# Kernel optimization log

Hardware: AMD Instinct MI355X
Metric: run time of the kernel (lower is better)

Reference implementation:

```python
import jax, jax.numpy as jnp
import numpy as np

B, H, L, D, BLK = 2, 16, 2048, 64, 32
NB = L // BLK          # 64 blocks per side
WINDOW = 8             # causal local window, in blocks


def make_layout():
    # [H, NB, NB] int32: block (i, j) active iff 0 <= i - j < WINDOW (causal local band)
    bi = jnp.arange(NB)
    band = ((bi[:, None] - bi[None, :]) >= 0) & ((bi[:, None] - bi[None, :]) < WINDOW)
    return jnp.broadcast_to(band[None].astype(jnp.int32), (H, NB, NB))


def setup_inputs() -> dict:
    rng = jax.random.key(0)
    kq, kk, kv, kp = jax.random.split(rng, 4)
    return {
        "query": jax.random.normal(kq, (B, H, L, D), dtype=jnp.float32),
        "key": jax.random.normal(kk, (B, H, L, D), dtype=jnp.float32),
        "value": jax.random.normal(kv, (B, H, L, D), dtype=jnp.float32),
        "key_padding_mask": jax.random.normal(kp, (B, L), dtype=jnp.float32),
        "layout": make_layout(),
    }


def reference(query, key, value, key_padding_mask, layout):
    # query/key/value: [B, H, L, D]; layout: [H, NB, NB] block sparsity pattern
    bsz, num_heads, tgt_len, head_dim = query.shape
    blk = tgt_len // layout.shape[1]
    scaling = float(head_dim) ** (-0.5)

    # SDD: scores only on active blocks. Reference computes dense then masks
    # inactive blocks to -inf, matching blocksparse softmax semantics exactly.
    scores = jnp.einsum("bhqd,bhkd->bhqk", query, key) * scaling
    # key_padding_mask_mode='add': added to logits, broadcast over queries
    scores = scores + key_padding_mask[:, None, None, :]

    # expand block layout [H, NB, NB] -> element mask [H, L, L]
    block_mask = jnp.repeat(jnp.repeat(layout.astype(bool), blk, axis=1), blk, axis=2)
    scores = jnp.where(block_mask[None], scores, -jnp.inf)

    probs = jax.nn.softmax(scores, axis=-1)  # zeros outside active blocks
    # DSD: probs @ value
    attn_output = jnp.einsum("bhqk,bhkd->bhqd", probs, value)
    return attn_output
```

## Files before the change

### kernel.cpp

```cpp
#include <hip/hip_runtime.h>

#define B_   2
#define H_   16
#define L_   2048
#define D_   64
#define BLK_ 32
#define NB_  64
#define WIN_ 8

#define KS 72
#define VS 40
#define PS 40

typedef __bf16 bf16x8 __attribute__((ext_vector_type(8)));
typedef float  f32x4  __attribute__((ext_vector_type(4)));
typedef unsigned short u16x4 __attribute__((ext_vector_type(4)));
typedef unsigned short u16x8 __attribute__((ext_vector_type(8)));

__device__ inline unsigned short f2bf(float f) {
    unsigned int u = __builtin_bit_cast(unsigned int, f);
    unsigned int r = u + 0x7fffu + ((u >> 16) & 1u);
    return (unsigned short)(r >> 16);
}

__global__ __launch_bounds__(256, 4)
void sparse_attn_kernel(const float* __restrict__ qg,
                        const float* __restrict__ kg,
                        const float* __restrict__ vg,
                        const float* __restrict__ kpm,
                        const int*   __restrict__ layout,
                        float* __restrict__ outg)
{
    __shared__ __align__(16) unsigned short Ks_[2][BLK_ * KS];
    __shared__ __align__(16) unsigned short Vt_[2][D_ * VS];
    __shared__ __align__(16) unsigned short Ps_[4][16 * PS];

    const int tid  = threadIdx.x;
    const int wave = tid >> 6;
    const int lane = tid & 63;
    const int quad = lane >> 4;
    const int l15  = lane & 15;

    const int phys = blockIdx.x;
    const int lw   = (phys & 7) * 128 + (phys >> 3);
    const int ip = lw & 31;
    const int h  = (lw >> 5) & 15;
    const int b  = lw >> 9;
    const int i0 = ip * 2, i1 = i0 + 1;
    const int iq = i0 + (wave >> 1);

    const size_t bh = (size_t)(b * H_ + h);
    const float* kbase  = kg  + bh * L_ * D_;
    const float* vbase  = vg  + bh * L_ * D_;
    const float* kpb    = kpm + (size_t)b * L_;
    const int*   layrow = layout + (h * NB_ + iq) * NB_;

    bf16x8 aq[2];
    {
        const int gq = iq * BLK_ + (wave & 1) * 16 + l15;
        const float* qrow = qg + (bh * L_ + gq) * D_;
        #pragma unroll
        for (int ks = 0; ks < 2; ++ks) {
            float4 x = *(const float4*)&qrow[ks * 32 + quad * 8];
            float4 y = *(const float4*)&qrow[ks * 32 + quad * 8 + 4];
            u16x8 pk;
            pk[0]=f2bf(x.x); pk[1]=f2bf(x.y); pk[2]=f2bf(x.z); pk[3]=f2bf(x.w);
            pk[4]=f2bf(y.x); pk[5]=f2bf(y.y); pk[6]=f2bf(y.z); pk[7]=f2bf(y.w);
            aq[ks] = __builtin_bit_cast(bf16x8, pk);
        }
    }

    int jlo = i0 - (WIN_ - 1);
    if (jlo < 0) jlo = 0;

    {
        const float4* kb = (const float4*)(kbase + (size_t)jlo * BLK_ * D_);
        float4 a0 = kb[tid];
        float4 a1 = kb[tid + 256];
        const float* vb = vbase + (size_t)jlo * BLK_ * D_;
        float vr[8];
        #pragma unroll
        for (int i = 0; i < 8; ++i) vr[i] = vb[(wave * 8 + i) * D_ + lane];
        {
            int row = tid >> 4, c4 = tid & 15;
            u16x4 pk; pk[0]=f2bf(a0.x); pk[1]=f2bf(a0.y); pk[2]=f2bf(a0.z); pk[3]=f2bf(a0.w);
            *(u16x4*)&Ks_[0][row * KS + c4 * 4] = pk;
            int f4 = tid + 256; row = f4 >> 4; c4 = f4 & 15;
            u16x4 pj; pj[0]=f2bf(a1.x); pj[1]=f2bf(a1.y); pj[2]=f2bf(a1.z); pj[3]=f2bf(a1.w);
            *(u16x4*)&Ks_[0][row * KS + c4 * 4] = pj;
        }
        {
            u16x8 pv;
            #pragma unroll
            for (int i = 0; i < 8; ++i) pv[i] = f2bf(vr[i]);
            *(u16x8*)&Vt_[0][lane * VS + ((wave ^ (lane & 3)) * 8)] = pv;
        }
    }
    float kp0c = kpb[jlo * BLK_ + l15];
    float kp1c = kpb[jlo * BLK_ + 16 + l15];
    __syncthreads();

    float lrow[4] = {0.f, 0.f, 0.f, 0.f};
    f32x4 Ot[4];
    #pragma unroll
    for (int t = 0; t < 4; ++t) Ot[t] = (f32x4){0.f, 0.f, 0.f, 0.f};

    int cur = 0;
    for (int j = jlo; j <= i1; ++j) {
        const bool havenext = (j < i1);
        float4 kr0, kr1; float vr[8];
        float kp0n = 0.f, kp1n = 0.f;
        if (havenext) {
            const float4* kb = (const float4*)(kbase + (size_t)(j + 1) * BLK_ * D_);
            kr0 = kb[tid]; kr1 = kb[tid + 256];
            const float* vb = vbase + (size_t)(j + 1) * BLK_ * D_;
            #pragma unroll
            for (int i = 0; i < 8; ++i) vr[i] = vb[(wave * 8 + i) * D_ + lane];
            kp0n = kpb[(j + 1) * BLK_ + l15];
            kp1n = kpb[(j + 1) * BLK_ + 16 + l15];
        }

        if (layrow[j] != 0) {
            f32x4 s0 = {0.f,0.f,0.f,0.f}, s1 = {0.f,0.f,0.f,0.f};
            #pragma unroll
            for (int ks = 0; ks < 2; ++ks) {
                bf16x8 b0 = *(const bf16x8*)&Ks_[cur][l15 * KS + ks * 32 + quad * 8];
                bf16x8 b1 = *(const bf16x8*)&Ks_[cur][(16 + l15) * KS + ks * 32 + quad * 8];
                s0 = __builtin_amdgcn_mfma_f32_16x16x32_bf16(aq[ks], b0, s0, 0, 0, 0);
                s1 = __builtin_amdgcn_mfma_f32_16x16x32_bf16(aq[ks], b1, s1, 0, 0, 0);
            }
            unsigned short* psw = &Ps_[wave][0];
            #pragma unroll
            for (int r = 0; r < 4; ++r) {
                float v0 = s0[r] * 0.125f + kp0c;
                float v1 = s1[r] * 0.125f + kp1c;
                float p0 = __expf(v0);
                float p1 = __expf(v1);
                lrow[r] += p0 + p1;
                int prow = quad * 4 + r;
                psw[prow * PS + l15]      = f2bf(p0);
                psw[prow * PS + 16 + l15] = f2bf(p1);
            }
            asm volatile("s_waitcnt lgkmcnt(0)" ::: "memory");
            bf16x8 ap = *(const bf16x8*)&psw[l15 * PS + quad * 8];
            #pragma unroll
            for (int t = 0; t < 4; ++t) {
                bf16x8 bv = *(const bf16x8*)&Vt_[cur][(t * 16 + l15) * VS + ((quad ^ (l15 & 3)) * 8)];
                Ot[t] = __builtin_amdgcn_mfma_f32_16x16x32_bf16(ap, bv, Ot[t], 0, 0, 0);
            }
        }

        if (havenext) {
            const int nb = cur ^ 1;
            int row = tid >> 4, c4 = tid & 15;
            u16x4 pk; pk[0]=f2bf(kr0.x); pk[1]=f2bf(kr0.y); pk[2]=f2bf(kr0.z); pk[3]=f2bf(kr0.w);
            *(u16x4*)&Ks_[nb][row * KS + c4 * 4] = pk;
            int f4 = tid + 256; row = f4 >> 4; c4 = f4 & 15;
            u16x4 pj; pj[0]=f2bf(kr1.x); pj[1]=f2bf(kr1.y); pj[2]=f2bf(kr1.z); pj[3]=f2bf(kr1.w);
            *(u16x4*)&Ks_[nb][row * KS + c4 * 4] = pj;
            u16x8 pv;
            #pragma unroll
            for (int i = 0; i < 8; ++i) pv[i] = f2bf(vr[i]);
            *(u16x8*)&Vt_[nb][lane * VS + ((wave ^ (lane & 3)) * 8)] = pv;
            kp0c = kp0n; kp1c = kp1n;
        }
        __syncthreads();
        cur ^= 1;
    }

    #pragma unroll
    for (int r = 0; r < 4; ++r) {
        #pragma unroll
        for (int m = 1; m < 16; m <<= 1) lrow[r] += __shfl_xor(lrow[r], m);
    }
    float* ob = outg + (bh * L_ + (size_t)iq * BLK_ + (wave & 1) * 16) * D_;
    #pragma unroll
    for (int r = 0; r < 4; ++r) {
        float inv = 1.0f / lrow[r];
        int prow = quad * 4 + r;
        #pragma unroll
        for (int t = 0; t < 4; ++t)
            ob[prow * D_ + t * 16 + l15] = Ot[t][r] * inv;
    }
}

extern "C" void kernel_launch(void* const* d_in, const int* in_sizes, int n_in,
                              void* d_out, int out_size, void* d_ws, size_t ws_size,
                              hipStream_t stream) {
    const float* q      = (const float*)d_in[0];
    const float* k      = (const float*)d_in[1];
    const float* v      = (const float*)d_in[2];
    const float* kpmask = (const float*)d_in[3];
    const int*   layout = (const int*)d_in[4];
    float* out = (float*)d_out;

    dim3 grid(B_ * H_ * (NB_ / 2));
    dim3 block(256);
    sparse_attn_kernel<<<grid, block, 0, stream>>>(q, k, v, kpmask, layout, out);
}
```

Before: 105.6 us.

## Fully unroll fixed 9-step block loop with two-deep register prefetch and XOR-swizzled K

```diff
diff --git a/kernel.cpp b/kernel.cpp
--- a/kernel.cpp
+++ b/kernel.cpp
@@ -6,15 +6,13 @@
 #define D_   64
 #define BLK_ 32
 #define NB_  64
-#define WIN_ 8
 
-#define KS 72
-#define VS 40
-#define PS 40
+#define KSW 64
+#define VS  40
+#define PS  40
 
 typedef __bf16 bf16x8 __attribute__((ext_vector_type(8)));
 typedef float  f32x4  __attribute__((ext_vector_type(4)));
-typedef unsigned short u16x4 __attribute__((ext_vector_type(4)));
 typedef unsigned short u16x8 __attribute__((ext_vector_type(8)));
 
 __device__ inline unsigned short f2bf(float f) {
@@ -22,6 +20,14 @@
     unsigned int r = u + 0x7fffu + ((u >> 16) & 1u);
     return (unsigned short)(r >> 16);
 }
+
+#define WG_BARRIER() asm volatile("s_waitcnt lgkmcnt(0)\n\ts_barrier" ::: "memory")
+
+struct Tile {
+    float4 k0, k1;
+    float  v[8];
+    float  kp0, kp1;
+};
 
 __global__ __launch_bounds__(256, 4)
 void sparse_attn_kernel(const float* __restrict__ qg,
@@ -31,7 +37,7 @@
                         const int*   __restrict__ layout,
                         float* __restrict__ outg)
 {
-    __shared__ __align__(16) unsigned short Ks_[2][BLK_ * KS];
+    __shared__ __align__(16) unsigned short Ks_[2][BLK_ * KSW];
     __shared__ __align__(16) unsigned short Vt_[2][D_ * VS];
     __shared__ __align__(16) unsigned short Ps_[4][16 * PS];
 
@@ -55,6 +61,15 @@
     const float* kpb    = kpm + (size_t)b * L_;
     const int*   layrow = layout + (h * NB_ + iq) * NB_;
 
+    const int jbeg = i0 - 7;
+
+    int act[9];
+    #pragma unroll
+    for (int s = 0; s < 9; ++s) {
+        const int j = jbeg + s;
+        act[s] = (j >= 0) ? layrow[j] : 0;
+    }
+
     bf16x8 aq[2];
     {
         const int gq = iq * BLK_ + (wave & 1) * 16 + l15;
@@ -70,101 +85,84 @@
         }
     }
 
-    int jlo = i0 - (WIN_ - 1);
-    if (jlo < 0) jlo = 0;
+    auto clampj = [&](int j) { return j < 0 ? 0 : j; };
 
-    {
-        const float4* kb = (const float4*)(kbase + (size_t)jlo * BLK_ * D_);
-        float4 a0 = kb[tid];
-        float4 a1 = kb[tid + 256];
-        const float* vb = vbase + (size_t)jlo * BLK_ * D_;
-        float vr[8];
+    auto loadT = [&](int jc, Tile& T) {
+        const float4* kb = (const float4*)(kbase + (size_t)jc * BLK_ * D_);
+        T.k0 = kb[tid * 2];
+        T.k1 = kb[tid * 2 + 1];
+        const float* vb = vbase + (size_t)jc * BLK_ * D_;
         #pragma unroll
-        for (int i = 0; i < 8; ++i) vr[i] = vb[(wave * 8 + i) * D_ + lane];
-        {
-            int row = tid >> 4, c4 = tid & 15;
-            u16x4 pk; pk[0]=f2bf(a0.x); pk[1]=f2bf(a0.y); pk[2]=f2bf(a0.z); pk[3]=f2bf(a0.w);
-            *(u16x4*)&Ks_[0][row * KS + c4 * 4] = pk;
-            int f4 = tid + 256; row = f4 >> 4; c4 = f4 & 15;
-            u16x4 pj; pj[0]=f2bf(a1.x); pj[1]=f2bf(a1.y); pj[2]=f2bf(a1.z); pj[3]=f2bf(a1.w);
-            *(u16x4*)&Ks_[0][row * KS + c4 * 4] = pj;
-        }
-        {
-            u16x8 pv;
-            #pragma unroll
-            for (int i = 0; i < 8; ++i) pv[i] = f2bf(vr[i]);
-            *(u16x8*)&Vt_[0][lane * VS + ((wave ^ (lane & 3)) * 8)] = pv;
-        }
-    }
-    float kp0c = kpb[jlo * BLK_ + l15];
-    float kp1c = kpb[jlo * BLK_ + 16 + l15];
-    __syncthreads();
+        for (int i = 0; i < 8; ++i) T.v[i] = vb[(wave * 8 + i) * D_ + lane];
+        T.kp0 = kpb[jc * BLK_ + l15];
+        T.kp1 = kpb[jc * BLK_ + 16 + l15];
+    };
+
+    auto storeT = [&](int buf, const Tile& T) {
+        const int row = tid >> 3, oct = tid & 7;
+        u16x8 pk;
+        pk[0]=f2bf(T.k0.x); pk[1]=f2bf(T.k0.y); pk[2]=f2bf(T.k0.z); pk[3]=f2bf(T.k0.w);
+        pk[4]=f2bf(T.k1.x); pk[5]=f2bf(T.k1.y); pk[6]=f2bf(T.k1.z); pk[7]=f2bf(T.k1.w);
+        *(u16x8*)&Ks_[buf][row * KSW + ((oct ^ (row & 7)) * 8)] = pk;
+        u16x8 pv;
+        #pragma unroll
+        for (int i = 0; i < 8; ++i) pv[i] = f2bf(T.v[i]);
+        *(u16x8*)&Vt_[buf][lane * VS + ((wave ^ (lane & 3)) * 8)] = pv;
+    };
 
     float lrow[4] = {0.f, 0.f, 0.f, 0.f};
     f32x4 Ot[4];
     #pragma unroll
     for (int t = 0; t < 4; ++t) Ot[t] = (f32x4){0.f, 0.f, 0.f, 0.f};
 
+    auto computeT = [&](int buf, float kp0c, float kp1c) {
+        f32x4 s0 = {0.f,0.f,0.f,0.f}, s1 = {0.f,0.f,0.f,0.f};
+        #pragma unroll
+        for (int ks = 0; ks < 2; ++ks) {
+            const int so = ((ks * 4 + quad) ^ (l15 & 7)) * 8;
+            bf16x8 b0 = *(const bf16x8*)&Ks_[buf][l15 * KSW + so];
+            bf16x8 b1 = *(const bf16x8*)&Ks_[buf][(16 + l15) * KSW + so];
+            s0 = __builtin_amdgcn_mfma_f32_16x16x32_bf16(aq[ks], b0, s0, 0, 0, 0);
+            s1 = __builtin_amdgcn_mfma_f32_16x16x32_bf16(aq[ks], b1, s1, 0, 0, 0);
+        }
+        unsigned short* psw = &Ps_[wave][0];
+        #pragma unroll
+        for (int r = 0; r < 4; ++r) {
+            float p0 = __expf(s0[r] * 0.125f + kp0c);
+            float p1 = __expf(s1[r] * 0.125f + kp1c);
+            lrow[r] += p0 + p1;
+            const int prow = quad * 4 + r;
+            psw[prow * PS + l15]      = f2bf(p0);
+            psw[prow * PS + 16 + l15] = f2bf(p1);
+        }
+        asm volatile("s_waitcnt lgkmcnt(0)" ::: "memory");
+        bf16x8 ap = *(const bf16x8*)&psw[l15 * PS + quad * 8];
+        #pragma unroll
+        for (int t = 0; t < 4; ++t) {
+            bf16x8 bv = *(const bf16x8*)&Vt_[buf][(t * 16 + l15) * VS + ((quad ^ (l15 & 3)) * 8)];
+            Ot[t] = __builtin_amdgcn_mfma_f32_16x16x32_bf16(ap, bv, Ot[t], 0, 0, 0);
+        }
+    };
+
+    Tile tiles[2];
+    loadT(clampj(jbeg), tiles[0]);
+    storeT(0, tiles[0]);
+    float kp0c = tiles[0].kp0, kp1c = tiles[0].kp1;
+    loadT(clampj(jbeg + 1), tiles[1]);
+    WG_BARRIER();
+
     int cur = 0;
-    for (int j = jlo; j <= i1; ++j) {
-        const bool havenext = (j < i1);
-        float4 kr0, kr1; float vr[8];
-        float kp0n = 0.f, kp1n = 0.f;
-        if (havenext) {
-            const float4* kb = (const float4*)(kbase + (size_t)(j + 1) * BLK_ * D_);
-            kr0 = kb[tid]; kr1 = kb[tid + 256];
-            const float* vb = vbase + (size_t)(j + 1) * BLK_ * D_;
-            #pragma unroll
-            for (int i = 0; i < 8; ++i) vr[i] = vb[(wave * 8 + i) * D_ + lane];
-            kp0n = kpb[(j + 1) * BLK_ + l15];
-            kp1n = kpb[(j + 1) * BLK_ + 16 + l15];
+    #pragma unroll
+    for (int s = 0; s < 9; ++s) {
+        const int j = jbeg + s;
+        if (s <= 6) loadT(clampj(j + 2), tiles[s & 1]);
+        if (act[s] != 0) computeT(cur, kp0c, kp1c);
+        if (s < 8) {
+            const Tile& T = tiles[(s + 1) & 1];
+            storeT(cur ^ 1, T);
+            kp0c = T.kp0; kp1c = T.kp1;
         }
-
-        if (layrow[j] != 0) {
-            f32x4 s0 = {0.f,0.f,0.f,0.f}, s1 = {0.f,0.f,0.f,0.f};
-            #pragma unroll
-            for (int ks = 0; ks < 2; ++ks) {
-                bf16x8 b0 = *(const bf16x8*)&Ks_[cur][l15 * KS + ks * 32 + quad * 8];
-                bf16x8 b1 = *(const bf16x8*)&Ks_[cur][(16 + l15) * KS + ks * 32 + quad * 8];
-                s0 = __builtin_amdgcn_mfma_f32_16x16x32_bf16(aq[ks], b0, s0, 0, 0, 0);
-                s1 = __builtin_amdgcn_mfma_f32_16x16x32_bf16(aq[ks], b1, s1, 0, 0, 0);
-            }
-            unsigned short* psw = &Ps_[wave][0];
-            #pragma unroll
-            for (int r = 0; r < 4; ++r) {
-                float v0 = s0[r] * 0.125f + kp0c;
-                float v1 = s1[r] * 0.125f + kp1c;
-                float p0 = __expf(v0);
-                float p1 = __expf(v1);
-                lrow[r] += p0 + p1;
-                int prow = quad * 4 + r;
-                psw[prow * PS + l15]      = f2bf(p0);
-                psw[prow * PS + 16 + l15] = f2bf(p1);
-            }
-            asm volatile("s_waitcnt lgkmcnt(0)" ::: "memory");
-            bf16x8 ap = *(const bf16x8*)&psw[l15 * PS + quad * 8];
-            #pragma unroll
-            for (int t = 0; t < 4; ++t) {
-                bf16x8 bv = *(const bf16x8*)&Vt_[cur][(t * 16 + l15) * VS + ((quad ^ (l15 & 3)) * 8)];
-                Ot[t] = __builtin_amdgcn_mfma_f32_16x16x32_bf16(ap, bv, Ot[t], 0, 0, 0);
-            }
-        }
-
-        if (havenext) {
-            const int nb = cur ^ 1;
-            int row = tid >> 4, c4 = tid & 15;
-            u16x4 pk; pk[0]=f2bf(kr0.x); pk[1]=f2bf(kr0.y); pk[2]=f2bf(kr0.z); pk[3]=f2bf(kr0.w);
-            *(u16x4*)&Ks_[nb][row * KS + c4 * 4] = pk;
-            int f4 = tid + 256; row = f4 >> 4; c4 = f4 & 15;
-            u16x4 pj; pj[0]=f2bf(kr1.x); pj[1]=f2bf(kr1.y); pj[2]=f2bf(kr1.z); pj[3]=f2bf(kr1.w);
-            *(u16x4*)&Ks_[nb][row * KS + c4 * 4] = pj;
-            u16x8 pv;
-            #pragma unroll
-            for (int i = 0; i < 8; ++i) pv[i] = f2bf(vr[i]);
-            *(u16x8*)&Vt_[nb][lane * VS + ((wave ^ (lane & 3)) * 8)] = pv;
-            kp0c = kp0n; kp1c = kp1n;
-        }
-        __syncthreads();
+        WG_BARRIER();
         cur ^= 1;
     }
 
```

New measurement: 102.8 us. 2.6% less time.
